# Performance work log

Hardware: AMD Instinct MI355X
Metric: run time of the kernel (lower is better)

## Reference

```python
import jax, jax.numpy as jnp
import numpy as np

B, N, D, H = 4, 2048, 1024, 16
DH = D // H


def setup_inputs() -> dict:
    key = jax.random.key(0)
    ks = jax.random.split(key, 9)
    s = 1.0 / np.sqrt(D)
    return {
        "x": jax.random.normal(ks[0], (B, N, D), dtype=jnp.float32),
        "Wq": jax.random.normal(ks[1], (D, D), dtype=jnp.float32) * s,
        "bq": jax.random.normal(ks[2], (D,), dtype=jnp.float32) * 0.01,
        "Wk": jax.random.normal(ks[3], (D, D), dtype=jnp.float32) * s,
        "bk": jax.random.normal(ks[4], (D,), dtype=jnp.float32) * 0.01,
        "Wv": jax.random.normal(ks[5], (D, D), dtype=jnp.float32) * s,
        "bv": jax.random.normal(ks[6], (D,), dtype=jnp.float32) * 0.01,
        "Wp": jax.random.normal(ks[7], (D, D), dtype=jnp.float32) * s,
        "bp": jax.random.normal(ks[8], (D,), dtype=jnp.float32) * 0.01,
    }


def reference(x, Wq, bq, Wk, bk, Wv, bv, Wp, bp):
    b, n, d = x.shape
    # torch Linear: x @ W.T + b; reshape to (b, h, n, dh)
    def heads(W, bias):
        y = jnp.einsum('bnd,ed->bne', x, W) + bias
        return y.reshape(b, n, H, DH).transpose(0, 2, 1, 3)
    q, k, v = heads(Wq, bq), heads(Wk, bk), heads(Wv, bv)
    # NOTE: source multiplies by sqrt(d_head) (bug in original), kept faithfully
    scale = jnp.sqrt(jnp.float32(DH))
    att = jnp.einsum('bhqd,bhkd->bhqk', q, k) * scale
    causal = jnp.triu(jnp.ones((n, n), dtype=bool), k=1)  # True above diagonal
    att = jnp.where(causal, -jnp.inf, att)
    att = jax.nn.softmax(att, axis=-1)
    # dropout is eval-mode identity
    out = jnp.einsum('bhqk,bhkd->bhqd', att, v)
    out = out.transpose(0, 2, 1, 3).reshape(b, n, d)
    return jnp.einsum('bnd,ed->bne', out, Wp) + bp
```

## Files before the change

kernel.cpp:

```cpp
#include <hip/hip_runtime.h>
#include <hip/hip_fp16.h>


typedef _Float16 half8 __attribute__((ext_vector_type(8)));
typedef _Float16 half4 __attribute__((ext_vector_type(4)));
typedef float f32x4 __attribute__((ext_vector_type(4)));
typedef unsigned int u32x4 __attribute__((ext_vector_type(4)));

#define DEV __device__ __forceinline__
#define MFMA16(a, b, c) __builtin_amdgcn_mfma_f32_16x16x32_f16(a, b, c, 0, 0, 0)

DEV void gload_lds16(const void* g, void* l) {
  __builtin_amdgcn_global_load_lds(
      (const __attribute__((address_space(1))) void*)g,
      (__attribute__((address_space(3))) void*)l, 16, 0, 0);
}

__global__ __launch_bounds__(256) void cast_all(
    const float* __restrict__ x, const float* __restrict__ Wq,
    const float* __restrict__ Wk, const float* __restrict__ Wv,
    const float* __restrict__ Wp, __half* __restrict__ xb,
    __half* __restrict__ wqkv, __half* __restrict__ wpb) {
  int i = blockIdx.x * 256 + threadIdx.x;
  const float* s;
  __half* d;
  int j;
  if (i < 1048576) {
    s = x; d = xb; j = i;
  } else {
    int k = i - 1048576;
    int sel = k >> 17;
    j = k & 131071;
    s = (sel == 0) ? Wq : (sel == 1) ? Wk : (sel == 2) ? Wv : Wp;
    d = (sel == 3) ? wpb : (wqkv + sel * 1048576);
  }
  const float4* sp = (const float4*)s + (size_t)j * 2;
  float4 a = sp[0], b = sp[1];
  half8 h;
  h[0] = (_Float16)a.x; h[1] = (_Float16)a.y; h[2] = (_Float16)a.z; h[3] = (_Float16)a.w;
  h[4] = (_Float16)b.x; h[5] = (_Float16)b.y; h[6] = (_Float16)b.z; h[7] = (_Float16)b.w;
  *((half8*)d + j) = h;
}

template <int MODE>
__global__ __launch_bounds__(256) void gemm128(
    const __half* __restrict__ A, const __half* __restrict__ Bm,
    const float* __restrict__ b0, const float* __restrict__ b1,
    const float* __restrict__ b2, __half* __restrict__ oh,
    __half* __restrict__ vtp, float* __restrict__ of) {
  const int m0 = blockIdx.y * 128;
  const int n0 = blockIdx.x * 128;
  const int tid = threadIdx.x;
  const int w = tid >> 6, lane = tid & 63;
  const int lr = lane & 15, lq = lane >> 4;
  const int wr = w >> 1, wc = w & 1;

  __shared__ alignas(16) __half As[128 * 64];
  __shared__ alignas(16) __half Bs[128 * 64];

  f32x4 acc[4][4] = {};

  const int arow = lane >> 3;
  const int acol = ((lane & 7) ^ arow) * 8;
  const __half* Agp = A + ((size_t)m0 + w * 32 + arow) * 1024 + acol;
  const __half* Bgp = Bm + ((size_t)n0 + w * 32 + arow) * 1024 + acol;

  for (int kt = 0; kt < 16; ++kt) {
#pragma unroll
    for (int j = 0; j < 4; ++j) {
      gload_lds16(Agp + j * 8192 + kt * 64, As + (w * 4 + j) * 512);
      gload_lds16(Bgp + j * 8192 + kt * 64, Bs + (w * 4 + j) * 512);
    }
    __syncthreads();
#pragma unroll
    for (int s = 0; s < 2; ++s) {
      half8 af[4], bf[4];
#pragma unroll
      for (int i = 0; i < 4; ++i) {
        int rowA = wr * 64 + i * 16 + lr;
        int rowB = wc * 64 + i * 16 + lr;
        af[i] = *(const half8*)((const char*)As +
                                ((rowA * 128 + s * 64 + lq * 16) ^ ((rowA & 7) << 4)));
        bf[i] = *(const half8*)((const char*)Bs +
                                ((rowB * 128 + s * 64 + lq * 16) ^ ((rowB & 7) << 4)));
      }
#pragma unroll
      for (int mi = 0; mi < 4; ++mi)
#pragma unroll
        for (int ni = 0; ni < 4; ++ni)
          acc[mi][ni] = MFMA16(af[mi], bf[ni], acc[mi][ni]);
    }
    __syncthreads();
  }

  if (MODE == 0) {
#pragma unroll
    for (int ni = 0; ni < 4; ++ni) {
      int col = n0 + wc * 64 + ni * 16 + lr;
      int t = col >> 10, e = col & 1023;
      const float* bb = (t == 0) ? b0 : ((t == 1) ? b1 : b2);
      float bias = bb[e];
      int hh = e >> 6, dh = e & 63;
      if (t == 2) {
#pragma unroll
        for (int mi = 0; mi < 4; ++mi) {
          int row = m0 + wr * 64 + mi * 16 + lq * 4;
          int b_ = row >> 11, n = row & 2047;
          half4 h;
#pragma unroll
          for (int r = 0; r < 4; ++r) h[r] = (_Float16)(acc[mi][ni][r] + bias);
          *(half4*)(vtp + (size_t)(b_ * 16 + hh) * 131072 + (size_t)dh * 2048 + n) = h;
        }
      } else {
        float scale = (t == 0) ? 11.541560327111707f : 1.0f;
        __half* base = oh + (size_t)t * 8388608 + dh;
#pragma unroll
        for (int mi = 0; mi < 4; ++mi)
#pragma unroll
          for (int r = 0; r < 4; ++r) {
            int row = m0 + wr * 64 + mi * 16 + lq * 4 + r;
            int b_ = row >> 11, n = row & 2047;
            float v = (acc[mi][ni][r] + bias) * scale;
            base[(((size_t)(b_ * 16 + hh) * 2048 + n) * 64)] = __float2half(v);
          }
      }
    }
  } else {
#pragma unroll
    for (int ni = 0; ni < 4; ++ni) {
      int col = n0 + wc * 64 + ni * 16 + lr;
      float bias = b0[col];
#pragma unroll
      for (int mi = 0; mi < 4; ++mi)
#pragma unroll
        for (int r = 0; r < 4; ++r) {
          int row = m0 + wr * 64 + mi * 16 + lq * 4 + r;
          of[(size_t)row * 1024 + col] = acc[mi][ni][r] + bias;
        }
    }
  }
}

__global__ __launch_bounds__(256, 3) void attn128(const __half* __restrict__ Q,
                                                  const __half* __restrict__ K,
                                                  const __half* __restrict__ Vt,
                                                  __half* __restrict__ O) {
  const int wg = blockIdx.x;
  const int bh = wg & 63;
  const int qt = 15 - (wg >> 6);
  const int b = bh >> 4, h = bh & 15;
  const int tid = threadIdx.x;
  const int w = tid >> 6, lane = tid & 63;
  const int lr = lane & 15, lq = lane >> 4;
  const int hi = lane >> 5;
  const int sAl = (lane & 15) | ((lane & 16) << 1);
  const int sBl = sAl + 16;

  __shared__ alignas(16) __half Ks[2][4096];
  __shared__ alignas(16) __half Vs[2][4096];

  const __half* Kb = K + (size_t)bh * 131072;
  const __half* Vb = Vt + (size_t)bh * 131072;

  const int srow0 = tid >> 3;
  const int srow1 = srow0 + 32;
  const int scol = ((tid & 7) ^ (srow0 & 7)) * 8;

#define STAGE(t, buf)                                                          \
  do {                                                                         \
    gload_lds16(Kb + (size_t)((t)*64 + srow0) * 64 + scol, Ks[buf] + tid * 8); \
    gload_lds16(Kb + (size_t)((t)*64 + srow1) * 64 + scol,                     \
                Ks[buf] + 2048 + tid * 8);                                     \
    gload_lds16(Vb + (size_t)srow0 * 2048 + (t)*64 + scol, Vs[buf] + tid * 8); \
    gload_lds16(Vb + (size_t)srow1 * 2048 + (t)*64 + scol,                     \
                Vs[buf] + 2048 + tid * 8);                                     \
  } while (0)

  const int q0 = qt * 128;
  const int ktend = 2 * qt + 2;
  const int rmin = q0 + w * 32;
  const int myqa = rmin + lr;
  const int myqb = rmin + 16 + lr;

  const __half* Qpa = Q + ((size_t)bh * 2048 + rmin) * 64;
  half8 qf0a = *(const half8*)(Qpa + lr * 64 + lq * 8);
  half8 qf1a = *(const half8*)(Qpa + lr * 64 + 32 + lq * 8);
  half8 qf0b = *(const half8*)(Qpa + (16 + lr) * 64 + lq * 8);
  half8 qf1b = *(const half8*)(Qpa + (16 + lr) * 64 + 32 + lq * 8);

  f32x4 oacca[4] = {}, oaccb[4] = {};
  float ma = -INFINITY, la = 0.f, mb = -INFINITY, lb = 0.f;

  STAGE(0, 0);
  asm volatile("" ::: "memory");

  auto smgrp = [&](f32x4* sacc, float& m, float& l, int myq, int k0,
                   bool needmask, f32x4* oacc, half8& pa0, half8& pa1) {
    if (needmask) {
#pragma unroll
      for (int nt = 0; nt < 4; ++nt)
#pragma unroll
        for (int r = 0; r < 4; ++r) {
          int key = k0 + nt * 16 + lq * 4 + r;
          if (key > myq) sacc[nt][r] = -INFINITY;
        }
    }
    float rm = fmaxf(sacc[0][0], sacc[0][1]);
    rm = fmaxf(fmaxf(rm, sacc[0][2]), sacc[0][3]);
    rm = fmaxf(fmaxf(rm, sacc[1][0]), sacc[1][1]);
    rm = fmaxf(fmaxf(rm, sacc[1][2]), sacc[1][3]);
    rm = fmaxf(fmaxf(rm, sacc[2][0]), sacc[2][1]);
    rm = fmaxf(fmaxf(rm, sacc[2][2]), sacc[2][3]);
    rm = fmaxf(fmaxf(rm, sacc[3][0]), sacc[3][1]);
    rm = fmaxf(fmaxf(rm, sacc[3][2]), sacc[3][3]);
    rm = fmaxf(rm, __shfl_xor(rm, 16));
    rm = fmaxf(rm, __shfl_xor(rm, 32));
    if (__any(rm > m + 8.f)) {
      float mn = fmaxf(m, rm);
      float al = __builtin_amdgcn_exp2f(m - mn);
      m = mn;
      l *= al;
      float al4[4];
#pragma unroll
      for (int r = 0; r < 4; ++r) al4[r] = __shfl(al, lq * 4 + r);
#pragma unroll
      for (int dt = 0; dt < 4; ++dt)
#pragma unroll
        for (int r = 0; r < 4; ++r) oacc[dt][r] *= al4[r];
    }
    float ps = 0.f;
#pragma unroll
    for (int nt = 0; nt < 4; ++nt) {
      float p0 = __builtin_amdgcn_exp2f(sacc[nt][0] - m);
      float p1 = __builtin_amdgcn_exp2f(sacc[nt][1] - m);
      float p2 = __builtin_amdgcn_exp2f(sacc[nt][2] - m);
      float p3 = __builtin_amdgcn_exp2f(sacc[nt][3] - m);
      sacc[nt][0] = p0; sacc[nt][1] = p1;
      sacc[nt][2] = p2; sacc[nt][3] = p3;
      ps += (p0 + p1) + (p2 + p3);
    }
    l += ps;
    unsigned ph[8];
#pragma unroll
    for (int nt = 0; nt < 4; ++nt) {
      __half2 pha = __floats2half2_rn(sacc[nt][0], sacc[nt][1]);
      __half2 phb = __floats2half2_rn(sacc[nt][2], sacc[nt][3]);
      ph[2 * nt] = *(unsigned*)&pha;
      ph[2 * nt + 1] = *(unsigned*)&phb;
    }
    u32x4 fa, fb;
    {
      unsigned t0, t1;
      t0 = __shfl((int)ph[0], sAl); t1 = __shfl((int)ph[2], sAl);
      fa[0] = hi ? t1 : t0;
      t0 = __shfl((int)ph[1], sAl); t1 = __shfl((int)ph[3], sAl);
      fa[1] = hi ? t1 : t0;
      t0 = __shfl((int)ph[0], sBl); t1 = __shfl((int)ph[2], sBl);
      fa[2] = hi ? t1 : t0;
      t0 = __shfl((int)ph[1], sBl); t1 = __shfl((int)ph[3], sBl);
      fa[3] = hi ? t1 : t0;
      t0 = __shfl((int)ph[4], sAl); t1 = __shfl((int)ph[6], sAl);
      fb[0] = hi ? t1 : t0;
      t0 = __shfl((int)ph[5], sAl); t1 = __shfl((int)ph[7], sAl);
      fb[1] = hi ? t1 : t0;
      t0 = __shfl((int)ph[4], sBl); t1 = __shfl((int)ph[6], sBl);
      fb[2] = hi ? t1 : t0;
      t0 = __shfl((int)ph[5], sBl); t1 = __shfl((int)ph[7], sBl);
      fb[3] = hi ? t1 : t0;
    }
    pa0 = *(half8*)&fa;
    pa1 = *(half8*)&fb;
  };

  for (int kt = 0; kt < ktend; ++kt) {
    const int cur = kt & 1;
    const int k0 = kt * 64;
    if (kt + 1 < ktend) {
      STAGE(kt + 1, cur ^ 1);
      asm volatile("s_waitcnt vmcnt(4)" ::: "memory");
    } else {
      asm volatile("s_waitcnt vmcnt(0)" ::: "memory");
    }
    __builtin_amdgcn_s_barrier();
    asm volatile("" ::: "memory");

    const char* Kc = (const char*)Ks[cur];
    const char* Vc = (const char*)Vs[cur];
    if (k0 <= rmin + 31) {
      f32x4 sa[4] = {}, sb[4] = {};
      __builtin_amdgcn_s_setprio(1);
#pragma unroll
      for (int nt = 0; nt < 4; ++nt) {
        int row = nt * 16 + lr;
        half8 kb0 = *(const half8*)(Kc + ((row * 128 + lq * 16) ^ ((row & 7) << 4)));
        half8 kb1 = *(const half8*)(Kc + ((row * 128 + 64 + lq * 16) ^ ((row & 7) << 4)));
        sa[nt] = MFMA16(kb0, qf0a, sa[nt]);
        sa[nt] = MFMA16(kb1, qf1a, sa[nt]);
        sb[nt] = MFMA16(kb0, qf0b, sb[nt]);
        sb[nt] = MFMA16(kb1, qf1b, sb[nt]);
      }
      __builtin_amdgcn_s_setprio(0);

      half8 paa0, paa1, pab0, pab1;
      smgrp(sa, ma, la, myqa, k0, k0 + 63 > rmin, oacca, paa0, paa1);
      smgrp(sb, mb, lb, myqb, k0, k0 + 63 > rmin + 16, oaccb, pab0, pab1);

      __builtin_amdgcn_s_setprio(1);
#pragma unroll
      for (int dt = 0; dt < 4; ++dt) {
        int row = dt * 16 + lr;
        half8 vb0 = *(const half8*)(Vc + ((row * 128 + lq * 16) ^ ((row & 7) << 4)));
        half8 vb1 = *(const half8*)(Vc + ((row * 128 + 64 + lq * 16) ^ ((row & 7) << 4)));
        oacca[dt] = MFMA16(paa0, vb0, oacca[dt]);
        oacca[dt] = MFMA16(paa1, vb1, oacca[dt]);
        oaccb[dt] = MFMA16(pab0, vb0, oaccb[dt]);
        oaccb[dt] = MFMA16(pab1, vb1, oaccb[dt]);
      }
      __builtin_amdgcn_s_setprio(0);
    }
    asm volatile("s_waitcnt lgkmcnt(0)" ::: "memory");
    __builtin_amdgcn_s_barrier();
    asm volatile("" ::: "memory");
  }

  auto epi = [&](f32x4* oacc, float lpart, int grow) {
    float lt = lpart;
    lt += __shfl_xor(lt, 16);
    lt += __shfl_xor(lt, 32);
    float linv = 1.0f / lt;
    float inv4[4];
#pragma unroll
    for (int r = 0; r < 4; ++r) inv4[r] = __shfl(linv, lq * 4 + r);
    __half* Op = O + ((size_t)b * 2048 + rmin + grow) * 1024 + h * 64;
#pragma unroll
    for (int dt = 0; dt < 4; ++dt)
#pragma unroll
      for (int r = 0; r < 4; ++r)
        Op[(size_t)(lq * 4 + r) * 1024 + dt * 16 + lr] =
            __float2half(oacc[dt][r] * inv4[r]);
  };
  epi(oacca, la, 0);
  epi(oaccb, lb, 16);
#undef STAGE
}

extern "C" void kernel_launch(void* const* d_in, const int* in_sizes, int n_in,
                              void* d_out, int out_size, void* d_ws,
                              size_t ws_size, hipStream_t stream) {
  const float* x = (const float*)d_in[0];
  const float* Wq = (const float*)d_in[1];
  const float* bq = (const float*)d_in[2];
  const float* Wk = (const float*)d_in[3];
  const float* bk = (const float*)d_in[4];
  const float* Wv = (const float*)d_in[5];
  const float* bv = (const float*)d_in[6];
  const float* Wp = (const float*)d_in[7];
  const float* bp = (const float*)d_in[8];

  char* ws = (char*)d_ws;
  const size_t XB = 0;
  const size_t WQKV = XB + 16777216;
  const size_t WPB = WQKV + 6291456;
  const size_t QKV = WPB + 2097152;
  const size_t VT = QKV + 50331648;
  const size_t OB = VT + 16777216;

  __half* xb = (__half*)(ws + XB);
  __half* wqkv = (__half*)(ws + WQKV);
  __half* wpb = (__half*)(ws + WPB);
  __half* qkv = (__half*)(ws + QKV);
  __half* vt = (__half*)(ws + VT);
  __half* ob = (__half*)(ws + OB);

  cast_all<<<6144, 256, 0, stream>>>(x, Wq, Wk, Wv, Wp, xb, wqkv, wpb);

  gemm128<0><<<dim3(24, 64), 256, 0, stream>>>(xb, wqkv, bq, bk, bv, qkv, vt,
                                               nullptr);
  attn128<<<dim3(1024), 256, 0, stream>>>(qkv, qkv + 8388608, vt, ob);
  gemm128<1><<<dim3(8, 64), 256, 0, stream>>>(ob, wpb, bp, nullptr, nullptr,
                                              nullptr, nullptr, (float*)d_out);
}
```

Before: 181.4 us.

## Replace LDS-staged 4-wave attention with single-wave blocks loading K/V directly

The attention kernel drops LDS double-buffering and barriers. Each 64-thread block handles one 32-row query tile and reads K and V^T fragments straight from global memory into MFMA operands. The goal is to remove barrier and LDS staging overhead and to tighten causal work granularity, with 4096 small blocks instead of 1024. In exchange, K/V reuse across waves moves from LDS to L2/L1 caches, and there is no software prefetch to hide global load latency.

```diff
diff --git a/kernel.cpp b/kernel.cpp
--- a/kernel.cpp
+++ b/kernel.cpp
@@ -141,44 +141,25 @@
   }
 }
 
-__global__ __launch_bounds__(256, 3) void attn128(const __half* __restrict__ Q,
-                                                  const __half* __restrict__ K,
-                                                  const __half* __restrict__ Vt,
-                                                  __half* __restrict__ O) {
+__global__ __launch_bounds__(64, 4) void attn_nl(const __half* __restrict__ Q,
+                                                 const __half* __restrict__ K,
+                                                 const __half* __restrict__ Vt,
+                                                 __half* __restrict__ O) {
   const int wg = blockIdx.x;
   const int bh = wg & 63;
-  const int qt = 15 - (wg >> 6);
+  const int t32 = 63 - (wg >> 6);
   const int b = bh >> 4, h = bh & 15;
-  const int tid = threadIdx.x;
-  const int w = tid >> 6, lane = tid & 63;
+  const int lane = threadIdx.x & 63;
   const int lr = lane & 15, lq = lane >> 4;
   const int hi = lane >> 5;
   const int sAl = (lane & 15) | ((lane & 16) << 1);
   const int sBl = sAl + 16;
 
-  __shared__ alignas(16) __half Ks[2][4096];
-  __shared__ alignas(16) __half Vs[2][4096];
-
   const __half* Kb = K + (size_t)bh * 131072;
   const __half* Vb = Vt + (size_t)bh * 131072;
 
-  const int srow0 = tid >> 3;
-  const int srow1 = srow0 + 32;
-  const int scol = ((tid & 7) ^ (srow0 & 7)) * 8;
-
-#define STAGE(t, buf)                                                          \
-  do {                                                                         \
-    gload_lds16(Kb + (size_t)((t)*64 + srow0) * 64 + scol, Ks[buf] + tid * 8); \
-    gload_lds16(Kb + (size_t)((t)*64 + srow1) * 64 + scol,                     \
-                Ks[buf] + 2048 + tid * 8);                                     \
-    gload_lds16(Vb + (size_t)srow0 * 2048 + (t)*64 + scol, Vs[buf] + tid * 8); \
-    gload_lds16(Vb + (size_t)srow1 * 2048 + (t)*64 + scol,                     \
-                Vs[buf] + 2048 + tid * 8);                                     \
-  } while (0)
-
-  const int q0 = qt * 128;
-  const int ktend = 2 * qt + 2;
-  const int rmin = q0 + w * 32;
+  const int rmin = t32 * 32;
+  const int ktend = t32 / 2 + 1;
   const int myqa = rmin + lr;
   const int myqb = rmin + 16 + lr;
 
@@ -190,9 +171,6 @@
 
   f32x4 oacca[4] = {}, oaccb[4] = {};
   float ma = -INFINITY, la = 0.f, mb = -INFINITY, lb = 0.f;
-
-  STAGE(0, 0);
-  asm volatile("" ::: "memory");
 
   auto smgrp = [&](f32x4* sacc, float& m, float& l, int myq, int k0,
                    bool needmask, f32x4* oacc, half8& pa0, half8& pa1) {
@@ -273,54 +251,33 @@
   };
 
   for (int kt = 0; kt < ktend; ++kt) {
-    const int cur = kt & 1;
     const int k0 = kt * 64;
-    if (kt + 1 < ktend) {
-      STAGE(kt + 1, cur ^ 1);
-      asm volatile("s_waitcnt vmcnt(4)" ::: "memory");
-    } else {
-      asm volatile("s_waitcnt vmcnt(0)" ::: "memory");
-    }
-    __builtin_amdgcn_s_barrier();
-    asm volatile("" ::: "memory");
-
-    const char* Kc = (const char*)Ks[cur];
-    const char* Vc = (const char*)Vs[cur];
-    if (k0 <= rmin + 31) {
-      f32x4 sa[4] = {}, sb[4] = {};
-      __builtin_amdgcn_s_setprio(1);
-#pragma unroll
-      for (int nt = 0; nt < 4; ++nt) {
-        int row = nt * 16 + lr;
-        half8 kb0 = *(const half8*)(Kc + ((row * 128 + lq * 16) ^ ((row & 7) << 4)));
-        half8 kb1 = *(const half8*)(Kc + ((row * 128 + 64 + lq * 16) ^ ((row & 7) << 4)));
-        sa[nt] = MFMA16(kb0, qf0a, sa[nt]);
-        sa[nt] = MFMA16(kb1, qf1a, sa[nt]);
-        sb[nt] = MFMA16(kb0, qf0b, sb[nt]);
-        sb[nt] = MFMA16(kb1, qf1b, sb[nt]);
-      }
-      __builtin_amdgcn_s_setprio(0);
-
-      half8 paa0, paa1, pab0, pab1;
-      smgrp(sa, ma, la, myqa, k0, k0 + 63 > rmin, oacca, paa0, paa1);
-      smgrp(sb, mb, lb, myqb, k0, k0 + 63 > rmin + 16, oaccb, pab0, pab1);
-
-      __builtin_amdgcn_s_setprio(1);
-#pragma unroll
-      for (int dt = 0; dt < 4; ++dt) {
-        int row = dt * 16 + lr;
-        half8 vb0 = *(const half8*)(Vc + ((row * 128 + lq * 16) ^ ((row & 7) << 4)));
-        half8 vb1 = *(const half8*)(Vc + ((row * 128 + 64 + lq * 16) ^ ((row & 7) << 4)));
-        oacca[dt] = MFMA16(paa0, vb0, oacca[dt]);
-        oacca[dt] = MFMA16(paa1, vb1, oacca[dt]);
-        oaccb[dt] = MFMA16(pab0, vb0, oaccb[dt]);
-        oaccb[dt] = MFMA16(pab1, vb1, oaccb[dt]);
-      }
-      __builtin_amdgcn_s_setprio(0);
-    }
-    asm volatile("s_waitcnt lgkmcnt(0)" ::: "memory");
-    __builtin_amdgcn_s_barrier();
-    asm volatile("" ::: "memory");
+    f32x4 sa[4] = {}, sb[4] = {};
+#pragma unroll
+    for (int nt = 0; nt < 4; ++nt) {
+      int row = k0 + nt * 16 + lr;
+      half8 kb0 = *(const half8*)(Kb + (size_t)row * 64 + lq * 8);
+      half8 kb1 = *(const half8*)(Kb + (size_t)row * 64 + 32 + lq * 8);
+      sa[nt] = MFMA16(kb0, qf0a, sa[nt]);
+      sa[nt] = MFMA16(kb1, qf1a, sa[nt]);
+      sb[nt] = MFMA16(kb0, qf0b, sb[nt]);
+      sb[nt] = MFMA16(kb1, qf1b, sb[nt]);
+    }
+
+    half8 paa0, paa1, pab0, pab1;
+    smgrp(sa, ma, la, myqa, k0, k0 + 63 > rmin, oacca, paa0, paa1);
+    smgrp(sb, mb, lb, myqb, k0, k0 + 63 > rmin + 16, oaccb, pab0, pab1);
+
+#pragma unroll
+    for (int dt = 0; dt < 4; ++dt) {
+      int row = dt * 16 + lr;
+      half8 vb0 = *(const half8*)(Vb + (size_t)row * 2048 + k0 + lq * 8);
+      half8 vb1 = *(const half8*)(Vb + (size_t)row * 2048 + k0 + 32 + lq * 8);
+      oacca[dt] = MFMA16(paa0, vb0, oacca[dt]);
+      oacca[dt] = MFMA16(paa1, vb1, oacca[dt]);
+      oaccb[dt] = MFMA16(pab0, vb0, oaccb[dt]);
+      oaccb[dt] = MFMA16(pab1, vb1, oaccb[dt]);
+    }
   }
 
   auto epi = [&](f32x4* oacc, float lpart, int grow) {
@@ -341,7 +298,6 @@
   };
   epi(oacca, la, 0);
   epi(oaccb, lb, 16);
-#undef STAGE
 }
 
 extern "C" void kernel_launch(void* const* d_in, const int* in_sizes, int n_in,
@@ -376,7 +332,7 @@
 
   gemm128<0><<<dim3(24, 64), 256, 0, stream>>>(xb, wqkv, bq, bk, bv, qkv, vt,
                                                nullptr);
-  attn128<<<dim3(1024), 256, 0, stream>>>(qkv, qkv + 8388608, vt, ob);
+  attn_nl<<<dim3(4096), 64, 0, stream>>>(qkv, qkv + 8388608, vt, ob);
   gemm128<1><<<dim3(8, 64), 256, 0, stream>>>(ob, wpb, bp, nullptr, nullptr,
                                               nullptr, nullptr, (float*)d_out);
 }
```

Result: slower. 247.0 us (+36.1%).
